# Performance work log

Hardware: AMD Instinct MI355X
Metric: run time of the kernel (lower is better)

The kernel has to match this reference:

```python
import jax, jax.numpy as jnp
import numpy as np
import math

NUM_HEADS = 16
D_MODEL = 1024
HEAD_DIM = D_MODEL // NUM_HEADS


def setup_inputs() -> dict:
    key = jax.random.key(0)
    k1, k2, k3 = jax.random.split(key, 3)
    x = jax.random.normal(k1, (4, 2048, D_MODEL), dtype=jnp.float32)
    # Linear(d_model, 3*d_model, bias=False): y = x @ w_qkv, w_qkv: [d_model, 3*d_model]
    w_qkv = jax.random.normal(k2, (D_MODEL, 3 * D_MODEL), dtype=jnp.float32) * (1.0 / math.sqrt(D_MODEL))
    w_o = jax.random.normal(k3, (D_MODEL, D_MODEL), dtype=jnp.float32) * (1.0 / math.sqrt(D_MODEL))
    return {"x": x, "w_qkv": w_qkv, "w_o": w_o}


def reference(x, w_qkv, w_o):
    B, S, _ = x.shape
    H, Dh = NUM_HEADS, HEAD_DIM
    qkv = (x @ w_qkv).reshape(B, S, 3, H, Dh)
    q = qkv[:, :, 0].transpose(0, 2, 1, 3)  # [B, H, S, Dh]
    k = qkv[:, :, 1].transpose(0, 2, 1, 3)
    v = qkv[:, :, 2].transpose(0, 2, 1, 3)
    scale = 1.0 / math.sqrt(Dh + 1e-9)
    scores = jnp.einsum("bhqd,bhkd->bhqk", q, k) * scale  # [B, H, S, S]
    probs = jax.nn.softmax(scores, axis=-1)
    # dropout is identity in eval mode
    out = jnp.einsum("bhqk,bhkd->bhqd", probs, v)  # [B, H, S, Dh]
    out = out.transpose(0, 2, 1, 3).reshape(B, S, H * Dh)
    return out @ w_o
```

## Files before the change

### kernel.cpp

```cpp
#include <hip/hip_runtime.h>
#include <hip/hip_bf16.h>

typedef __bf16 bf16_t;
typedef __bf16 bf16x8 __attribute__((ext_vector_type(8)));
typedef float f32x4 __attribute__((ext_vector_type(4)));
typedef unsigned int uint32x2 __attribute__((ext_vector_type(2)));
typedef unsigned int uint32x4 __attribute__((ext_vector_type(4)));

#define B_SZ 4
#define SEQ 2048
#define NH 16
#define DH 64
#define DM 1024
#define RSQ (3 * DM)

__device__ __forceinline__ void gload_lds16(const bf16_t* g, bf16_t* l) {
  __builtin_amdgcn_global_load_lds(
      (const __attribute__((address_space(1))) unsigned int*)g,
      (__attribute__((address_space(3))) unsigned int*)l, 16, 0, 0);
}

__device__ __forceinline__ unsigned lds_b32addr(void* p) {
  return (unsigned)(uintptr_t)(__attribute__((address_space(3))) void*)p;
}

__global__ __launch_bounds__(256) void f32_to_bf16_kernel(
    const float* __restrict__ in, bf16_t* __restrict__ out, int n) {
  int i = (blockIdx.x * blockDim.x + threadIdx.x) * 4;
  if (i >= n) return;
  float4 v = *reinterpret_cast<const float4*>(in + i);
  bf16_t o[4] = {(bf16_t)v.x, (bf16_t)v.y, (bf16_t)v.z, (bf16_t)v.w};
  *reinterpret_cast<uint2*>(out + i) = *reinterpret_cast<const uint2*>(o);
}

__global__ __launch_bounds__(256) void transpose_f32_bf16_kernel(
    const float* __restrict__ in, bf16_t* __restrict__ outT, int K, int N,
    int scale_cols, float scale) {
  __shared__ float tile[32][33];
  const int tx = threadIdx.x & 31;
  const int ty = threadIdx.x >> 5;
  const int n0 = blockIdx.x * 32;
  const int k0 = blockIdx.y * 32;
#pragma unroll
  for (int j = 0; j < 4; ++j)
    tile[ty + j * 8][tx] = in[(size_t)(k0 + ty + j * 8) * N + n0 + tx];
  __syncthreads();
#pragma unroll
  for (int j = 0; j < 4; ++j) {
    int n = n0 + ty + j * 8;
    float s = (n < scale_cols) ? scale : 1.0f;
    outT[(size_t)n * K + k0 + tx] = (bf16_t)(tile[tx][ty + j * 8] * s);
  }
}

template <typename OutT>
__global__ __launch_bounds__(256) void gemm_bt_kernel(
    const bf16_t* __restrict__ A, const bf16_t* __restrict__ Bt,
    OutT* __restrict__ C, int M, int N, int K) {
  __shared__ __align__(16) bf16_t As[128 * 64];
  __shared__ __align__(16) bf16_t Bs[128 * 64];

  const int tid = threadIdx.x;
  const int lane = tid & 63;
  const int wid = tid >> 6;
  const int l16 = lane & 15;
  const int g4 = lane >> 4;
  const int m0 = blockIdx.y * 128;
  const int n0 = blockIdx.x * 128;
  const int wm = (wid >> 1) * 64;
  const int wn = (wid & 1) * 64;

  const int srow = wid * 8 + (lane >> 3);
  const int scol = (lane & 7) * 8;
  const bf16_t* ap = A + (size_t)(m0 + srow) * K + scol;
  const bf16_t* bp = Bt + (size_t)(n0 + srow) * K + scol;

  f32x4 acc[4][4] = {};

  for (int k0 = 0; k0 < K; k0 += 64) {
    __syncthreads();
#pragma unroll
    for (int t = 0; t < 4; ++t) {
      gload_lds16(ap + k0 + (size_t)t * 32 * K, &As[(t * 32 + wid * 8) * 64]);
      gload_lds16(bp + k0 + (size_t)t * 32 * K, &Bs[(t * 32 + wid * 8) * 64]);
    }
    __syncthreads();

#pragma unroll
    for (int ks = 0; ks < 2; ++ks) {
      bf16x8 af[4], bfm[4];
#pragma unroll
      for (int i = 0; i < 4; ++i)
        af[i] = *reinterpret_cast<const bf16x8*>(
            &As[(wm + i * 16 + l16) * 64 + ks * 32 + g4 * 8]);
#pragma unroll
      for (int i = 0; i < 4; ++i)
        bfm[i] = *reinterpret_cast<const bf16x8*>(
            &Bs[(wn + i * 16 + l16) * 64 + ks * 32 + g4 * 8]);
#pragma unroll
      for (int mi = 0; mi < 4; ++mi)
#pragma unroll
        for (int ni = 0; ni < 4; ++ni)
          acc[mi][ni] = __builtin_amdgcn_mfma_f32_16x16x32_bf16(
              af[mi], bfm[ni], acc[mi][ni], 0, 0, 0);
    }
  }

#pragma unroll
  for (int mi = 0; mi < 4; ++mi)
#pragma unroll
    for (int ni = 0; ni < 4; ++ni)
#pragma unroll
      for (int r = 0; r < 4; ++r) {
        int row = m0 + wm + mi * 16 + g4 * 4 + r;
        int col = n0 + wn + ni * 16 + l16;
        C[(size_t)row * N + col] = (OutT)acc[mi][ni][r];
      }
}

template <bool PRE>
__device__ __forceinline__ void attn_body(
    const bf16_t* kp, const bf16_t* vp_next, bf16_t* vst_next, unsigned vrd,
    const bf16x8 (&qf)[4][2], f32x4 (&acc_o)[16], float (&lsum)[4]) {
  uint32x4 kf[2][2];
#pragma unroll
  for (int half = 0; half < 2; ++half)
#pragma unroll
    for (int kh = 0; kh < 2; ++kh)
      asm volatile("global_load_dwordx4 %0, %1, off"
                   : "=v"(kf[half][kh])
                   : "v"(kp + (size_t)half * 64 * RSQ + kh * 32)
                   : "memory");

  if constexpr (PRE) {
#pragma unroll
    for (int t = 0; t < 4; ++t)
      gload_lds16(vp_next + t * 16, vst_next + t * 512);
  }

  if constexpr (PRE)
    asm volatile("s_waitcnt vmcnt(8)" ::: "memory");
  else
    asm volatile("s_waitcnt vmcnt(4)" ::: "memory");

  uint32x2 vr[4][2];
#define TRR(dst, OFFSTR)                              \
  asm volatile("ds_read_b64_tr_b16 %0, %1 offset:" OFFSTR \
               : "=v"(dst)                            \
               : "v"(vrd))
  TRR(vr[0][0], "0");    TRR(vr[0][1], "512");
  TRR(vr[1][0], "1024"); TRR(vr[1][1], "1536");
  TRR(vr[2][0], "2048"); TRR(vr[2][1], "2560");
  TRR(vr[3][0], "3072"); TRR(vr[3][1], "3584");
#undef TRR

  if constexpr (PRE)
    asm volatile("s_waitcnt vmcnt(4)" ::: "memory");
  else
    asm volatile("s_waitcnt vmcnt(0)" ::: "memory");
  __builtin_amdgcn_sched_barrier(0);

  f32x4 sA[4] = {}, sB[4] = {};
#pragma unroll
  for (int qb = 0; qb < 4; ++qb) {
    sA[qb] = __builtin_amdgcn_mfma_f32_16x16x32_bf16(
        __builtin_bit_cast(bf16x8, kf[0][0]), qf[qb][0], sA[qb], 0, 0, 0);
    sA[qb] = __builtin_amdgcn_mfma_f32_16x16x32_bf16(
        __builtin_bit_cast(bf16x8, kf[0][1]), qf[qb][1], sA[qb], 0, 0, 0);
    sB[qb] = __builtin_amdgcn_mfma_f32_16x16x32_bf16(
        __builtin_bit_cast(bf16x8, kf[1][0]), qf[qb][0], sB[qb], 0, 0, 0);
    sB[qb] = __builtin_amdgcn_mfma_f32_16x16x32_bf16(
        __builtin_bit_cast(bf16x8, kf[1][1]), qf[qb][1], sB[qb], 0, 0, 0);
  }

  bf16x8 pf[4];
#pragma unroll
  for (int qb = 0; qb < 4; ++qb) {
    float p0 = __builtin_amdgcn_exp2f(sA[qb][0]);
    float p1 = __builtin_amdgcn_exp2f(sA[qb][1]);
    float p2 = __builtin_amdgcn_exp2f(sA[qb][2]);
    float p3 = __builtin_amdgcn_exp2f(sA[qb][3]);
    float p4 = __builtin_amdgcn_exp2f(sB[qb][0]);
    float p5 = __builtin_amdgcn_exp2f(sB[qb][1]);
    float p6 = __builtin_amdgcn_exp2f(sB[qb][2]);
    float p7 = __builtin_amdgcn_exp2f(sB[qb][3]);
    lsum[qb] += ((p0 + p1) + (p2 + p3)) + ((p4 + p5) + (p6 + p7));
    pf[qb][0] = (bf16_t)p0; pf[qb][1] = (bf16_t)p1;
    pf[qb][2] = (bf16_t)p2; pf[qb][3] = (bf16_t)p3;
    pf[qb][4] = (bf16_t)p4; pf[qb][5] = (bf16_t)p5;
    pf[qb][6] = (bf16_t)p6; pf[qb][7] = (bf16_t)p7;
  }

  asm volatile("s_waitcnt lgkmcnt(0)" ::: "memory");
  __builtin_amdgcn_sched_barrier(0);
  bf16x8 vf[4];
#pragma unroll
  for (int db = 0; db < 4; ++db) {
    uint32x4 c = {vr[db][0].x, vr[db][0].y, vr[db][1].x, vr[db][1].y};
    vf[db] = __builtin_bit_cast(bf16x8, c);
  }
#pragma unroll
  for (int qb = 0; qb < 4; ++qb)
#pragma unroll
    for (int db = 0; db < 4; ++db)
      acc_o[qb * 4 + db] = __builtin_amdgcn_mfma_f32_16x16x32_bf16(
          pf[qb], vf[db], acc_o[qb * 4 + db], 0, 0, 0);
}

__global__ __launch_bounds__(256) void attn_kernel(
    const bf16_t* __restrict__ qkv, bf16_t* __restrict__ out) {
  __shared__ __align__(16) unsigned char smem[33792];
  bf16_t* Vlds = (bf16_t*)smem;
  float(*Obuf)[66] = (float(*)[66])smem;
  float* lbuf = (float*)(smem + 32768);

  const int tid = threadIdx.x;
  const int lane = tid & 63;
  const int wid = tid >> 6;
  const int l16 = lane & 15;
  const int g4 = lane >> 4;

  const int D = blockIdx.x;
  const int g = ((D >> 8) << 3) + (D & 7);
  const int h = g & 15;
  const int b = g >> 4;
  const int q0 = ((D >> 3) & 31) * 64;

  const size_t base = (size_t)b * SEQ * RSQ;

  bf16x8 qf[4][2];
#pragma unroll
  for (int qb = 0; qb < 4; ++qb)
#pragma unroll
    for (int kh = 0; kh < 2; ++kh)
      qf[qb][kh] = __builtin_bit_cast(
          bf16x8, *reinterpret_cast<const uint4*>(
                      qkv + base + (size_t)(q0 + qb * 16 + l16) * RSQ + h * DH +
                      kh * 32 + g4 * 8));

  const bf16_t* kbase =
      qkv + base + (size_t)(wid * 16 + l16) * RSQ + DM + h * DH + g4 * 8;

  const int keyoff = ((lane >> 5) << 6) + wid * 16 + (((lane >> 3) & 3) << 2) +
                     ((lane >> 1) & 3);
  const bf16_t* vsrc =
      qkv + base + (size_t)keyoff * RSQ + 2 * DM + h * DH + (lane & 1) * 8;
  bf16_t* vwave = Vlds + wid * 4096;
  const unsigned vlane = lds_b32addr(vwave) + (lane << 3);

  f32x4 acc_o[16] = {};
  float lsum[4] = {0.f, 0.f, 0.f, 0.f};

#pragma unroll
  for (int t = 0; t < 4; ++t) gload_lds16(vsrc + t * 16, vwave + t * 512);

  for (int i = 0; i < 15; ++i) {
    const bf16_t* kp = kbase + (size_t)i * 128 * RSQ;
    const bf16_t* vp_next = vsrc + (size_t)(i + 1) * 128 * RSQ;
    bf16_t* vst_next = vwave + ((i + 1) & 1) * 2048;
    unsigned vrd = vlane + (i & 1) * 4096;
    attn_body<true>(kp, vp_next, vst_next, vrd, qf, acc_o, lsum);
  }
  attn_body<false>(kbase + (size_t)15 * 128 * RSQ, nullptr, nullptr,
                   vlane + 4096, qf, acc_o, lsum);

#pragma unroll
  for (int qb = 0; qb < 4; ++qb) {
    float t = lsum[qb];
    t += __shfl_xor(t, 16, 64);
    t += __shfl_xor(t, 32, 64);
    if (g4 == 0) lbuf[wid * 64 + qb * 16 + l16] = t;
  }

  for (int ph = 0; ph < 4; ++ph) {
    __syncthreads();
    if (wid == ph) {
#pragma unroll
      for (int qb = 0; qb < 4; ++qb)
#pragma unroll
        for (int db = 0; db < 4; ++db)
#pragma unroll
          for (int r = 0; r < 4; ++r) {
            int q = qb * 16 + g4 * 4 + r;
            int d = db * 16 + l16;
            if (ph == 0)
              Obuf[q][d] = acc_o[qb * 4 + db][r];
            else
              Obuf[q][d] += acc_o[qb * 4 + db][r];
          }
    }
  }
  __syncthreads();

  {
    int q = wid * 16 + l16;
    float l = lbuf[0 * 64 + q] + lbuf[1 * 64 + q] + lbuf[2 * 64 + q] +
              lbuf[3 * 64 + q];
    float inv = 1.f / l;
    bf16_t ob[16];
#pragma unroll
    for (int c = 0; c < 16; ++c)
      ob[c] = (bf16_t)(Obuf[q][g4 * 16 + c] * inv);
    bf16_t* op = out + (size_t)(b * SEQ + q0 + q) * DM + h * DH + g4 * 16;
    *reinterpret_cast<uint4*>(op) = *reinterpret_cast<const uint4*>(&ob[0]);
    *reinterpret_cast<uint4*>(op + 8) = *reinterpret_cast<const uint4*>(&ob[8]);
  }
}

extern "C" void kernel_launch(void* const* d_in, const int* in_sizes, int n_in,
                              void* d_out, int out_size, void* d_ws, size_t ws_size,
                              hipStream_t stream) {
  const float* x = (const float*)d_in[0];
  const float* w_qkv = (const float*)d_in[1];
  const float* w_o = (const float*)d_in[2];
  float* out = (float*)d_out;

  bf16_t* xb = (bf16_t*)d_ws;
  bf16_t* wqkvt = xb + (size_t)8192 * 1024;
  bf16_t* wot = wqkvt + (size_t)3072 * 1024;
  bf16_t* qkv = wot + (size_t)1024 * 1024;
  bf16_t* attn = qkv + (size_t)8192 * 3072;

  dim3 blk(256);
  const float c_exp2 = 0.18033688011112042f;

  f32_to_bf16_kernel<<<8192, blk, 0, stream>>>(x, xb, 8192 * 1024);
  transpose_f32_bf16_kernel<<<dim3(3072 / 32, 1024 / 32), blk, 0, stream>>>(
      w_qkv, wqkvt, 1024, 3072, 1024, c_exp2);
  transpose_f32_bf16_kernel<<<dim3(1024 / 32, 1024 / 32), blk, 0, stream>>>(
      w_o, wot, 1024, 1024, 0, 1.0f);

  gemm_bt_kernel<bf16_t><<<dim3(3072 / 128, 8192 / 128), blk, 0, stream>>>(
      xb, wqkvt, qkv, 8192, 3072, 1024);
  attn_kernel<<<2048, blk, 0, stream>>>(qkv, attn);
  gemm_bt_kernel<float><<<dim3(1024 / 128, 8192 / 128), blk, 0, stream>>>(
      attn, wot, out, 8192, 1024, 1024);
}
```

Before: 233.6 us.

## Double-buffer K fragments across iterations and compute row sums via MFMA

K tile loads are now issued one iteration ahead into a ping-pong register pair, so the score MFMAs no longer wait on the current iteration's global loads. The loop is unrolled by two to swap buffers, and the last iteration issues dummy wraparound loads that are drained afterwards. The per-lane exp-sum additions and end-of-loop shuffles are replaced by an extra MFMA against a ones vector that accumulates the row sums of the bf16-rounded probabilities. This trades VALU adds for MFMA work, raises register pressure, and slightly changes the normalisation numerics.

```diff
diff --git a/kernel.cpp b/kernel.cpp
--- a/kernel.cpp
+++ b/kernel.cpp
@@ -118,77 +118,62 @@
       }
 }
 
-template <bool PRE>
 __device__ __forceinline__ void attn_body(
-    const bf16_t* kp, const bf16_t* vp_next, bf16_t* vst_next, unsigned vrd,
-    const bf16x8 (&qf)[4][2], f32x4 (&acc_o)[16], float (&lsum)[4]) {
-  uint32x4 kf[2][2];
+    const bf16_t* kp_next, const bf16_t* vp_next, bf16_t* vst_next,
+    unsigned vrd_cur, uint32x4 (&kf_use)[2][2], uint32x4 (&kf_load)[2][2],
+    const bf16x8 (&qf)[4][2], const bf16x8 vones, f32x4 (&acc_o)[16],
+    f32x4 (&acc_l)[4]) {
 #pragma unroll
   for (int half = 0; half < 2; ++half)
 #pragma unroll
     for (int kh = 0; kh < 2; ++kh)
       asm volatile("global_load_dwordx4 %0, %1, off"
-                   : "=v"(kf[half][kh])
-                   : "v"(kp + (size_t)half * 64 * RSQ + kh * 32)
+                   : "=v"(kf_load[half][kh])
+                   : "v"(kp_next + (size_t)half * 64 * RSQ + kh * 32)
                    : "memory");
 
-  if constexpr (PRE) {
-#pragma unroll
-    for (int t = 0; t < 4; ++t)
-      gload_lds16(vp_next + t * 16, vst_next + t * 512);
-  }
-
-  if constexpr (PRE)
-    asm volatile("s_waitcnt vmcnt(8)" ::: "memory");
-  else
-    asm volatile("s_waitcnt vmcnt(4)" ::: "memory");
+#pragma unroll
+  for (int t = 0; t < 4; ++t)
+    gload_lds16(vp_next + t * 16, vst_next + t * 512);
+
+  asm volatile("s_waitcnt vmcnt(8)" ::: "memory");
+  __builtin_amdgcn_sched_barrier(0);
 
   uint32x2 vr[4][2];
 #define TRR(dst, OFFSTR)                              \
   asm volatile("ds_read_b64_tr_b16 %0, %1 offset:" OFFSTR \
                : "=v"(dst)                            \
-               : "v"(vrd))
+               : "v"(vrd_cur))
   TRR(vr[0][0], "0");    TRR(vr[0][1], "512");
   TRR(vr[1][0], "1024"); TRR(vr[1][1], "1536");
   TRR(vr[2][0], "2048"); TRR(vr[2][1], "2560");
   TRR(vr[3][0], "3072"); TRR(vr[3][1], "3584");
 #undef TRR
 
-  if constexpr (PRE)
-    asm volatile("s_waitcnt vmcnt(4)" ::: "memory");
-  else
-    asm volatile("s_waitcnt vmcnt(0)" ::: "memory");
-  __builtin_amdgcn_sched_barrier(0);
-
   f32x4 sA[4] = {}, sB[4] = {};
 #pragma unroll
   for (int qb = 0; qb < 4; ++qb) {
     sA[qb] = __builtin_amdgcn_mfma_f32_16x16x32_bf16(
-        __builtin_bit_cast(bf16x8, kf[0][0]), qf[qb][0], sA[qb], 0, 0, 0);
+        __builtin_bit_cast(bf16x8, kf_use[0][0]), qf[qb][0], sA[qb], 0, 0, 0);
     sA[qb] = __builtin_amdgcn_mfma_f32_16x16x32_bf16(
-        __builtin_bit_cast(bf16x8, kf[0][1]), qf[qb][1], sA[qb], 0, 0, 0);
+        __builtin_bit_cast(bf16x8, kf_use[0][1]), qf[qb][1], sA[qb], 0, 0, 0);
     sB[qb] = __builtin_amdgcn_mfma_f32_16x16x32_bf16(
-        __builtin_bit_cast(bf16x8, kf[1][0]), qf[qb][0], sB[qb], 0, 0, 0);
+        __builtin_bit_cast(bf16x8, kf_use[1][0]), qf[qb][0], sB[qb], 0, 0, 0);
     sB[qb] = __builtin_amdgcn_mfma_f32_16x16x32_bf16(
-        __builtin_bit_cast(bf16x8, kf[1][1]), qf[qb][1], sB[qb], 0, 0, 0);
+        __builtin_bit_cast(bf16x8, kf_use[1][1]), qf[qb][1], sB[qb], 0, 0, 0);
   }
 
   bf16x8 pf[4];
 #pragma unroll
   for (int qb = 0; qb < 4; ++qb) {
-    float p0 = __builtin_amdgcn_exp2f(sA[qb][0]);
-    float p1 = __builtin_amdgcn_exp2f(sA[qb][1]);
-    float p2 = __builtin_amdgcn_exp2f(sA[qb][2]);
-    float p3 = __builtin_amdgcn_exp2f(sA[qb][3]);
-    float p4 = __builtin_amdgcn_exp2f(sB[qb][0]);
-    float p5 = __builtin_amdgcn_exp2f(sB[qb][1]);
-    float p6 = __builtin_amdgcn_exp2f(sB[qb][2]);
-    float p7 = __builtin_amdgcn_exp2f(sB[qb][3]);
-    lsum[qb] += ((p0 + p1) + (p2 + p3)) + ((p4 + p5) + (p6 + p7));
-    pf[qb][0] = (bf16_t)p0; pf[qb][1] = (bf16_t)p1;
-    pf[qb][2] = (bf16_t)p2; pf[qb][3] = (bf16_t)p3;
-    pf[qb][4] = (bf16_t)p4; pf[qb][5] = (bf16_t)p5;
-    pf[qb][6] = (bf16_t)p6; pf[qb][7] = (bf16_t)p7;
+    pf[qb][0] = (bf16_t)__builtin_amdgcn_exp2f(sA[qb][0]);
+    pf[qb][1] = (bf16_t)__builtin_amdgcn_exp2f(sA[qb][1]);
+    pf[qb][2] = (bf16_t)__builtin_amdgcn_exp2f(sA[qb][2]);
+    pf[qb][3] = (bf16_t)__builtin_amdgcn_exp2f(sA[qb][3]);
+    pf[qb][4] = (bf16_t)__builtin_amdgcn_exp2f(sB[qb][0]);
+    pf[qb][5] = (bf16_t)__builtin_amdgcn_exp2f(sB[qb][1]);
+    pf[qb][6] = (bf16_t)__builtin_amdgcn_exp2f(sB[qb][2]);
+    pf[qb][7] = (bf16_t)__builtin_amdgcn_exp2f(sB[qb][3]);
   }
 
   asm volatile("s_waitcnt lgkmcnt(0)" ::: "memory");
@@ -200,11 +185,14 @@
     vf[db] = __builtin_bit_cast(bf16x8, c);
   }
 #pragma unroll
-  for (int qb = 0; qb < 4; ++qb)
+  for (int qb = 0; qb < 4; ++qb) {
+    acc_l[qb] = __builtin_amdgcn_mfma_f32_16x16x32_bf16(
+        pf[qb], vones, acc_l[qb], 0, 0, 0);
 #pragma unroll
     for (int db = 0; db < 4; ++db)
       acc_o[qb * 4 + db] = __builtin_amdgcn_mfma_f32_16x16x32_bf16(
           pf[qb], vf[db], acc_o[qb * 4 + db], 0, 0, 0);
+  }
 }
 
 __global__ __launch_bounds__(256) void attn_kernel(
@@ -248,28 +236,41 @@
   bf16_t* vwave = Vlds + wid * 4096;
   const unsigned vlane = lds_b32addr(vwave) + (lane << 3);
 
+  bf16x8 vones;
+#pragma unroll
+  for (int e = 0; e < 8; ++e) vones[e] = (bf16_t)1.0f;
+
   f32x4 acc_o[16] = {};
-  float lsum[4] = {0.f, 0.f, 0.f, 0.f};
-
+  f32x4 acc_l[4] = {};
+  uint32x4 kfA[2][2], kfB[2][2];
+
+#pragma unroll
+  for (int half = 0; half < 2; ++half)
+#pragma unroll
+    for (int kh = 0; kh < 2; ++kh)
+      asm volatile("global_load_dwordx4 %0, %1, off"
+                   : "=v"(kfA[half][kh])
+                   : "v"(kbase + (size_t)half * 64 * RSQ + kh * 32)
+                   : "memory");
 #pragma unroll
   for (int t = 0; t < 4; ++t) gload_lds16(vsrc + t * 16, vwave + t * 512);
 
-  for (int i = 0; i < 15; ++i) {
-    const bf16_t* kp = kbase + (size_t)i * 128 * RSQ;
-    const bf16_t* vp_next = vsrc + (size_t)(i + 1) * 128 * RSQ;
-    bf16_t* vst_next = vwave + ((i + 1) & 1) * 2048;
-    unsigned vrd = vlane + (i & 1) * 4096;
-    attn_body<true>(kp, vp_next, vst_next, vrd, qf, acc_o, lsum);
-  }
-  attn_body<false>(kbase + (size_t)15 * 128 * RSQ, nullptr, nullptr,
-                   vlane + 4096, qf, acc_o, lsum);
-
-#pragma unroll
-  for (int qb = 0; qb < 4; ++qb) {
-    float t = lsum[qb];
-    t += __shfl_xor(t, 16, 64);
-    t += __shfl_xor(t, 32, 64);
-    if (g4 == 0) lbuf[wid * 64 + qb * 16 + l16] = t;
+  for (int i = 0; i < 16; i += 2) {
+    const int i1 = (i + 1) & 15;
+    const int i2 = (i + 2) & 15;
+    attn_body(kbase + (size_t)i1 * 128 * RSQ, vsrc + (size_t)i1 * 128 * RSQ,
+              vwave + 2048, vlane, kfA, kfB, qf, vones, acc_o, acc_l);
+    attn_body(kbase + (size_t)i2 * 128 * RSQ, vsrc + (size_t)i2 * 128 * RSQ,
+              vwave, vlane + 4096, kfB, kfA, qf, vones, acc_o, acc_l);
+  }
+  asm volatile("s_waitcnt vmcnt(0)" ::: "memory");
+
+  if (l16 == 0) {
+#pragma unroll
+    for (int qb = 0; qb < 4; ++qb)
+#pragma unroll
+      for (int r = 0; r < 4; ++r)
+        lbuf[wid * 64 + qb * 16 + g4 * 4 + r] = acc_l[qb][r];
   }
 
   for (int ph = 0; ph < 4; ++ph) {
```

Result: slower. 251.4 us (+7.6%).

## Rewrite GEMMs as 8-wave double-buffered pipelined kernel with 128x256 tiles

Applied to the files above, without the earlier changes.

Replaces the 256-thread 128x128 GEMM with a 512-thread kernel that computes 128x256 tiles. It double-buffers the LDS tiles and splits the B-tile loads into halves so global-to-LDS prefetch of the next K tile overlaps the MFMA work. It also adds XCD-aware block swizzling and raises wave priority during MFMA sections. The cost is more LDS per block, finer-grained barriers, and manual vmcnt accounting that must match the issued load counts exactly.

```diff
diff --git a/kernel.cpp b/kernel.cpp
--- a/kernel.cpp
+++ b/kernel.cpp
@@ -54,67 +54,137 @@
 }
 
 template <typename OutT>
-__global__ __launch_bounds__(256) void gemm_bt_kernel(
+__global__ __launch_bounds__(512, 2) void gemm8p_kernel(
     const bf16_t* __restrict__ A, const bf16_t* __restrict__ Bt,
-    OutT* __restrict__ C, int M, int N, int K) {
-  __shared__ __align__(16) bf16_t As[128 * 64];
-  __shared__ __align__(16) bf16_t Bs[128 * 64];
+    OutT* __restrict__ C, int M, int N, int K, int NB) {
+  __shared__ __align__(16) bf16_t As[2][128 * 64];
+  __shared__ __align__(16) bf16_t Bs[2][256 * 64];
 
   const int tid = threadIdx.x;
   const int lane = tid & 63;
   const int wid = tid >> 6;
   const int l16 = lane & 15;
   const int g4 = lane >> 4;
-  const int m0 = blockIdx.y * 128;
-  const int n0 = blockIdx.x * 128;
-  const int wm = (wid >> 1) * 64;
-  const int wn = (wid & 1) * 64;
-
-  const int srow = wid * 8 + (lane >> 3);
-  const int scol = (lane & 7) * 8;
-  const bf16_t* ap = A + (size_t)(m0 + srow) * K + scol;
-  const bf16_t* bp = Bt + (size_t)(n0 + srow) * K + scol;
+  const int wm = wid >> 2;
+  const int wn = wid & 3;
+  const int tiles = K >> 6;
+
+  const int nwg = gridDim.x;
+  const int bid = blockIdx.x;
+  const int swz = (bid & 7) * (nwg >> 3) + (bid >> 3);
+  const int m0 = (swz / NB) * 128;
+  const int n0 = (swz % NB) * 256;
+
+  const bf16_t* aglob = A + (size_t)(m0 + (tid >> 3)) * K + (tid & 7) * 8;
+
+  auto stageA = [&](int t) {
+    int tt = (t == tiles) ? 0 : t;
+    int k0 = tt * 64;
+    int buf = tt & 1;
+#pragma unroll
+    for (int i = 0; i < 2; ++i)
+      gload_lds16(aglob + (size_t)i * 64 * K + k0,
+                  &As[buf][i * 4096 + wid * 512]);
+  };
+  auto stageB = [&](int t, int h) {
+    int tt = (t == tiles) ? 0 : t;
+    int k0 = tt * 64;
+    int buf = tt & 1;
+#pragma unroll
+    for (int j = 0; j < 2; ++j) {
+      int wrow = (2 * j + (wid >> 2)) * 64 + (wid & 3) * 8 + h * 32;
+      gload_lds16(
+          Bt + (size_t)(n0 + wrow + (lane >> 3)) * K + k0 + (lane & 7) * 8,
+          &Bs[buf][wrow * 64]);
+    }
+  };
 
   f32x4 acc[4][4] = {};
 
-  for (int k0 = 0; k0 < K; k0 += 64) {
-    __syncthreads();
-#pragma unroll
-    for (int t = 0; t < 4; ++t) {
-      gload_lds16(ap + k0 + (size_t)t * 32 * K, &As[(t * 32 + wid * 8) * 64]);
-      gload_lds16(bp + k0 + (size_t)t * 32 * K, &Bs[(t * 32 + wid * 8) * 64]);
-    }
-    __syncthreads();
-
-#pragma unroll
-    for (int ks = 0; ks < 2; ++ks) {
-      bf16x8 af[4], bfm[4];
-#pragma unroll
-      for (int i = 0; i < 4; ++i)
-        af[i] = *reinterpret_cast<const bf16x8*>(
-            &As[(wm + i * 16 + l16) * 64 + ks * 32 + g4 * 8]);
-#pragma unroll
-      for (int i = 0; i < 4; ++i)
-        bfm[i] = *reinterpret_cast<const bf16x8*>(
-            &Bs[(wn + i * 16 + l16) * 64 + ks * 32 + g4 * 8]);
-#pragma unroll
-      for (int mi = 0; mi < 4; ++mi)
-#pragma unroll
-        for (int ni = 0; ni < 4; ++ni)
-          acc[mi][ni] = __builtin_amdgcn_mfma_f32_16x16x32_bf16(
-              af[mi], bfm[ni], acc[mi][ni], 0, 0, 0);
-    }
-  }
-
-#pragma unroll
-  for (int mi = 0; mi < 4; ++mi)
-#pragma unroll
-    for (int ni = 0; ni < 4; ++ni)
+  stageA(0);
+  stageB(0, 0);
+  stageB(0, 1);
+  asm volatile("s_waitcnt vmcnt(2)" ::: "memory");
+  __builtin_amdgcn_s_barrier();
+  __builtin_amdgcn_sched_barrier(0);
+
+#pragma unroll 2
+  for (int t = 0; t < tiles; ++t) {
+    const int buf = t & 1;
+    const int abase = (wm * 64 + l16) * 64 + g4 * 8;
+    const int bbase = (wn * 64 + l16) * 64 + g4 * 8;
+
+    bf16x8 af[4][2], bf[2][2];
+#pragma unroll
+    for (int m = 0; m < 4; ++m)
+#pragma unroll
+      for (int ks = 0; ks < 2; ++ks)
+        af[m][ks] = *reinterpret_cast<const bf16x8*>(
+            &As[buf][abase + m * 16 * 64 + ks * 32]);
+#pragma unroll
+    for (int n = 0; n < 2; ++n)
+#pragma unroll
+      for (int ks = 0; ks < 2; ++ks)
+        bf[n][ks] = *reinterpret_cast<const bf16x8*>(
+            &Bs[buf][bbase + n * 16 * 64 + ks * 32]);
+
+    stageA(t + 1);
+    stageB(t + 1, 0);
+    asm volatile("s_waitcnt vmcnt(4)" ::: "memory");
+    __builtin_amdgcn_s_barrier();
+    __builtin_amdgcn_sched_barrier(0);
+
+    __builtin_amdgcn_s_setprio(1);
+#pragma unroll
+    for (int m = 0; m < 4; ++m)
+#pragma unroll
+      for (int n = 0; n < 2; ++n)
+#pragma unroll
+        for (int ks = 0; ks < 2; ++ks)
+          acc[m][n] = __builtin_amdgcn_mfma_f32_16x16x32_bf16(
+              af[m][ks], bf[n][ks], acc[m][n], 0, 0, 0);
+    __builtin_amdgcn_s_setprio(0);
+    __builtin_amdgcn_s_barrier();
+    __builtin_amdgcn_sched_barrier(0);
+
+    bf16x8 bg[2][2];
+#pragma unroll
+    for (int n = 0; n < 2; ++n)
+#pragma unroll
+      for (int ks = 0; ks < 2; ++ks)
+        bg[n][ks] = *reinterpret_cast<const bf16x8*>(
+            &Bs[buf][bbase + (n + 2) * 16 * 64 + ks * 32]);
+
+    stageB(t + 1, 1);
+    asm volatile("s_waitcnt vmcnt(2)" ::: "memory");
+    __builtin_amdgcn_s_barrier();
+    __builtin_amdgcn_sched_barrier(0);
+
+    __builtin_amdgcn_s_setprio(1);
+#pragma unroll
+    for (int m = 0; m < 4; ++m)
+#pragma unroll
+      for (int n = 0; n < 2; ++n)
+#pragma unroll
+        for (int ks = 0; ks < 2; ++ks)
+          acc[m][n + 2] = __builtin_amdgcn_mfma_f32_16x16x32_bf16(
+              af[m][ks], bg[n][ks], acc[m][n + 2], 0, 0, 0);
+    __builtin_amdgcn_s_setprio(0);
+    __builtin_amdgcn_s_barrier();
+    __builtin_amdgcn_sched_barrier(0);
+  }
+
+  asm volatile("s_waitcnt vmcnt(0)" ::: "memory");
+
+#pragma unroll
+  for (int m = 0; m < 4; ++m)
+#pragma unroll
+    for (int n = 0; n < 4; ++n)
 #pragma unroll
       for (int r = 0; r < 4; ++r) {
-        int row = m0 + wm + mi * 16 + g4 * 4 + r;
-        int col = n0 + wn + ni * 16 + l16;
-        C[(size_t)row * N + col] = (OutT)acc[mi][ni][r];
+        int row = m0 + wm * 64 + m * 16 + g4 * 4 + r;
+        int col = n0 + wn * 64 + n * 16 + l16;
+        C[(size_t)row * N + col] = (OutT)acc[m][n][r];
       }
 }
 
@@ -321,18 +391,17 @@
   bf16_t* qkv = wot + (size_t)1024 * 1024;
   bf16_t* attn = qkv + (size_t)8192 * 3072;
 
-  dim3 blk(256);
   const float c_exp2 = 0.18033688011112042f;
 
-  f32_to_bf16_kernel<<<8192, blk, 0, stream>>>(x, xb, 8192 * 1024);
-  transpose_f32_bf16_kernel<<<dim3(3072 / 32, 1024 / 32), blk, 0, stream>>>(
+  f32_to_bf16_kernel<<<8192, 256, 0, stream>>>(x, xb, 8192 * 1024);
+  transpose_f32_bf16_kernel<<<dim3(3072 / 32, 1024 / 32), 256, 0, stream>>>(
       w_qkv, wqkvt, 1024, 3072, 1024, c_exp2);
-  transpose_f32_bf16_kernel<<<dim3(1024 / 32, 1024 / 32), blk, 0, stream>>>(
+  transpose_f32_bf16_kernel<<<dim3(1024 / 32, 1024 / 32), 256, 0, stream>>>(
       w_o, wot, 1024, 1024, 0, 1.0f);
 
-  gemm_bt_kernel<bf16_t><<<dim3(3072 / 128, 8192 / 128), blk, 0, stream>>>(
-      xb, wqkvt, qkv, 8192, 3072, 1024);
-  attn_kernel<<<2048, blk, 0, stream>>>(qkv, attn);
-  gemm_bt_kernel<float><<<dim3(1024 / 128, 8192 / 128), blk, 0, stream>>>(
-      attn, wot, out, 8192, 1024, 1024);
-}
+  gemm8p_kernel<bf16_t><<<768, 512, 0, stream>>>(
+      xb, wqkvt, qkv, 8192, 3072, 1024, 12);
+  attn_kernel<<<2048, 256, 0, stream>>>(qkv, attn);
+  gemm8p_kernel<float><<<256, 512, 0, stream>>>(
+      attn, wot, out, 8192, 1024, 1024, 4);
+}
```

Result: no change. 233.5 us (-0.0%).
